# Performance work log

Measured on AMD Instinct MI355X. Metric: run time of the kernel, lower is better.

## Reference

```python
import jax, jax.numpy as jnp
import numpy as np

B, S, E, H = 4, 2048, 512, 1024

def setup_inputs() -> dict:
    key = jax.random.key(0)
    ks = jax.random.split(key, 8)
    s = 1.0 / np.sqrt(H)
    return {
        "hidden_states": jax.random.normal(ks[0], (B, S, H), jnp.float32),
        "external_embeddings": jax.random.normal(ks[1], (B, E, H), jnp.float32),
        "Wq": jax.random.normal(ks[2], (H, H), jnp.float32) * s,
        "bq": jax.random.normal(ks[3], (H,), jnp.float32) * 0.02,
        "Wk": jax.random.normal(ks[4], (H, H), jnp.float32) * s,
        "bk": jax.random.normal(ks[5], (H,), jnp.float32) * 0.02,
        "Wv": jax.random.normal(ks[6], (H, H), jnp.float32) * s,
        "bv": jax.random.normal(ks[7], (H,), jnp.float32) * 0.02,
    }

def reference(hidden_states, external_embeddings, Wq, bq, Wk, bk, Wv, bv):
    # Projections (torch Linear semantics: here weights stored as [in,out])
    q = hidden_states @ Wq + bq              # [B,S,H]
    k_tok = hidden_states @ Wk + bk          # [B,S,H]
    v_tok = hidden_states @ Wv + bv          # [B,S,H]
    k_ext = external_embeddings @ Wk + bk    # [B,E,H]
    v_ext = external_embeddings @ Wv + bv    # [B,E,H]
    # Each token attends to [its own key] ++ [external keys]; NO 1/sqrt(d) scaling
    # and NO head splitting, matching the original forward exactly.
    s_self = jnp.einsum('bsh,bsh->bs', q, k_tok)[..., None]   # [B,S,1]
    s_ext = jnp.einsum('bsh,beh->bse', q, k_ext)              # [B,S,E]
    scores = jnp.concatenate([s_self, s_ext], axis=-1)        # [B,S,1+E]
    probs = jax.nn.softmax(scores, axis=-1)
    ctx = probs[..., :1] * v_tok + jnp.einsum('bse,beh->bsh', probs[..., 1:], v_ext)
    return ctx  # [B,S,H]
```

## Files before the change

kernel.cpp:

```cpp
#include <hip/hip_runtime.h>
#include <stdint.h>

#define BB 4
#define SS 2048
#define EE 512
#define HH 1024

typedef _Float16 f16;
typedef __attribute__((ext_vector_type(8))) _Float16 f16x8;
typedef __attribute__((ext_vector_type(4))) _Float16 f16x4;
typedef __attribute__((ext_vector_type(4))) float f32x4;

__device__ __forceinline__ void async16(void* lds, const void* g) {
  __builtin_amdgcn_global_load_lds(
      (const __attribute__((address_space(1))) unsigned int*)g,
      (__attribute__((address_space(3))) unsigned int*)lds, 16, 0, 0);
}

template <int TERMS>
__device__ __forceinline__ void gemm_core(
    const f16* Ah, const f16* Al, const f16* Bh, const f16* Bl, int K, int ld,
    f16* lAh, f16* lAl, f16* lBh, f16* lBl, f32x4 acc[4][4]) {
  const int tid = threadIdx.x;
  const int wave = tid >> 6;
  const int lane = tid & 63;
  const int lrow = lane >> 2;
  const int lcol = (((lane & 3) ^ ((lane >> 3) & 3))) * 8;
  const int waveM = (wave >> 1) * 64;
  const int waveN = (wave & 1) * 64;
  const int frow = lane & 15;
  const int fk = ((lane >> 4) ^ ((frow >> 1) & 3)) * 8;

  for (int k0 = 0; k0 < K; k0 += 32) {
    __syncthreads();
#pragma unroll
    for (int i = 0; i < 2; ++i) {
      const int r0 = (wave * 2 + i) * 16;
      const size_t goff = (size_t)(r0 + lrow) * ld + (k0 + lcol);
      async16(&lAh[r0 * 32], Ah + goff);
      async16(&lBh[r0 * 32], Bh + goff);
      if (TERMS >= 2) async16(&lBl[r0 * 32], Bl + goff);
      if (TERMS >= 3) async16(&lAl[r0 * 32], Al + goff);
    }
    __syncthreads();

    f16x8 a[4], bh[4], bl[4], al[4];
#pragma unroll
    for (int i = 0; i < 4; ++i) {
      a[i] = *(const f16x8*)&lAh[(waveM + i * 16 + frow) * 32 + fk];
      bh[i] = *(const f16x8*)&lBh[(waveN + i * 16 + frow) * 32 + fk];
      if (TERMS >= 2) bl[i] = *(const f16x8*)&lBl[(waveN + i * 16 + frow) * 32 + fk];
      if (TERMS >= 3) al[i] = *(const f16x8*)&lAl[(waveM + i * 16 + frow) * 32 + fk];
    }
#pragma unroll
    for (int i = 0; i < 4; ++i)
#pragma unroll
      for (int j = 0; j < 4; ++j) {
        acc[i][j] = __builtin_amdgcn_mfma_f32_16x16x32_f16(a[i], bh[j], acc[i][j], 0, 0, 0);
        if (TERMS >= 2)
          acc[i][j] = __builtin_amdgcn_mfma_f32_16x16x32_f16(a[i], bl[j], acc[i][j], 0, 0, 0);
        if (TERMS >= 3)
          acc[i][j] = __builtin_amdgcn_mfma_f32_16x16x32_f16(al[i], bh[j], acc[i][j], 0, 0, 0);
      }
  }
}

__device__ __forceinline__ void epi_transposed(
    f16* __restrict__ dst, const f32x4 acc[4][4], const float bias[4], f16* tl) {
  const int tid = threadIdx.x, wave = tid >> 6, lane = tid & 63;
  const int waveM = (wave >> 1) * 64;
  const int colIn16 = lane & 15, quad = lane >> 4;
#pragma unroll
  for (int p = 0; p < 2; ++p) {
    __syncthreads();
    if ((wave & 1) == p) {
#pragma unroll
      for (int i = 0; i < 4; ++i)
#pragma unroll
        for (int j = 0; j < 4; ++j)
#pragma unroll
          for (int r = 0; r < 4; ++r) {
            const int row = waveM + i * 16 + quad * 4 + r;
            const int colL = j * 16 + colIn16;
            tl[colL * 136 + row] = (f16)(acc[i][j][r] + bias[j]);
          }
    }
    __syncthreads();
    for (int c = tid; c < 1024; c += 256) {
      const int colL = c >> 4, ch = c & 15;
      const f16x8 v = *(const f16x8*)&tl[colL * 136 + ch * 8];
      *(f16x8*)&dst[(size_t)(p * 64 + colL) * EE + ch * 8] = v;
    }
  }
}

__global__ __launch_bounds__(256) void cast_kernel(const float* __restrict__ xh32,
                                                   const float* __restrict__ xe32,
                                                   f16* __restrict__ xh,
                                                   f16* __restrict__ xe) {
  const int i = blockIdx.x * 256 + threadIdx.x;
  const int n4h = 8192 * HH / 4;
  const float* src = i < n4h ? xh32 : xe32;
  f16* dst = i < n4h ? xh : xe;
  const int k = i < n4h ? i : i - n4h;
  const float4 v = ((const float4*)src)[k];
  f16x4 o;
  o.x = (f16)v.x; o.y = (f16)v.y; o.z = (f16)v.z; o.w = (f16)v.w;
  ((f16x4*)dst)[k] = o;
}

__global__ void wsplit_kernel(const float* __restrict__ Wq, const float* __restrict__ Wk,
                              const float* __restrict__ Wv, f16* __restrict__ wt_hi,
                              f16* __restrict__ wt_lo) {
  __shared__ float tile[32][33];
  const int k0 = blockIdx.x * 32;
  const int n0g = blockIdx.y * 32;
  const int which = n0g >> 10;
  const float* W = which == 0 ? Wq : (which == 1 ? Wk : Wv);
  const int n0 = n0g & 1023;
  const int tx = threadIdx.x, ty = threadIdx.y;
#pragma unroll
  for (int i = 0; i < 32; i += 8)
    tile[ty + i][tx] = W[(size_t)(k0 + ty + i) * 1024 + n0 + tx];
  __syncthreads();
#pragma unroll
  for (int i = 0; i < 32; i += 8) {
    const int np = n0g + ty + i;
    const float v = tile[tx][ty + i];
    const size_t idx = (size_t)np * 1024 + k0 + tx;
    const f16 h = (f16)v;
    wt_hi[idx] = h;
    wt_lo[idx] = (f16)(v - (float)h);
  }
}

__global__ __launch_bounds__(256, 4) void proj_kernel(
    const f16* __restrict__ xh, const f16* __restrict__ xe,
    const f16* __restrict__ wt_hi, const f16* __restrict__ wt_lo,
    const float* __restrict__ bq, const float* __restrict__ bk,
    const float* __restrict__ bv, f16* __restrict__ q_hi, f16* __restrict__ q_lo,
    f16* __restrict__ kt, f16* __restrict__ vt,
    f16* __restrict__ ke_hi, f16* __restrict__ ke_lo, f16* __restrict__ veT) {
  const int g = blockIdx.x;
  const int j = g & 7;
  const int s = g >> 3;
  int mtile, ntile;
  if (s < 192) {
    const int w = s / 16, r = s % 16;
    ntile = w * 2 + (r & 1);
    mtile = (r >> 1) * 8 + j;
  } else {
    const int s2 = s - 192;
    const int w = s2 >> 2, r = s2 & 3;
    ntile = 8 + w * 2 + (r & 1);
    mtile = 64 + (r >> 1) * 8 + j;
  }
  const bool extRows = (mtile >= 64);

  __shared__ f16 lds[3 * 4096];

  const f16* A = extRows ? xe : xh;
  const int rowA = (extRows ? (mtile - 64) : mtile) * 128;
  const int rowB = ntile * 128;
  const bool split = (ntile < 8) || (extRows && ntile < 16);

  f32x4 acc[4][4];
#pragma unroll
  for (int i = 0; i < 4; ++i)
#pragma unroll
    for (int jj = 0; jj < 4; ++jj)
#pragma unroll
      for (int r = 0; r < 4; ++r) acc[i][jj][r] = 0.0f;

  if (split)
    gemm_core<2>(A + (size_t)rowA * HH, nullptr, wt_hi + (size_t)rowB * HH,
                 wt_lo + (size_t)rowB * HH, HH, HH,
                 lds, nullptr, lds + 4096, lds + 8192, acc);
  else
    gemm_core<1>(A + (size_t)rowA * HH, nullptr, wt_hi + (size_t)rowB * HH,
                 nullptr, HH, HH, lds, nullptr, lds + 4096, nullptr, acc);

  const int tid = threadIdx.x, wave = tid >> 6, lane = tid & 63;
  const int waveM = (wave >> 1) * 64, waveN = (wave & 1) * 64;
  const int colIn16 = lane & 15, rowQuad = (lane >> 4) * 4;
  float bias[4];
#pragma unroll
  for (int jj = 0; jj < 4; ++jj) {
    const int c = ntile * 128 + waveN + jj * 16 + colIn16;
    bias[jj] = c < 1024 ? bq[c] : (c < 2048 ? bk[c - 1024] : bv[c - 2048]);
  }

  if (extRows && ntile >= 16) {
    const int ge0 = (mtile - 64) * 128;
    const int bb = ge0 >> 9, e0 = ge0 & 511;
    epi_transposed(veT + ((size_t)bb * HH + (ntile - 16) * 128) * EE + e0,
                   acc, bias, lds);
    return;
  }

#pragma unroll
  for (int jj = 0; jj < 4; ++jj) {
    const int c = ntile * 128 + waveN + jj * 16 + colIn16;
#pragma unroll
    for (int i = 0; i < 4; ++i) {
#pragma unroll
      for (int r = 0; r < 4; ++r) {
        const int lrowIdx = waveM + i * 16 + rowQuad + r;
        const float val = acc[i][jj][r] + bias[jj];
        if (c < 1024) {
          const size_t idx = (size_t)(mtile * 128 + lrowIdx) * HH + c;
          const f16 h = (f16)val;
          q_hi[idx] = h;
          q_lo[idx] = (f16)(val - (float)h);
        } else if (c < 2048) {
          const int c2 = c - 1024;
          if (!extRows) {
            kt[(size_t)(mtile * 128 + lrowIdx) * HH + c2] = (f16)val;
          } else {
            const int ge = (mtile - 64) * 128 + lrowIdx;
            const size_t idx = (size_t)ge * HH + c2;
            const f16 h = (f16)val;
            ke_hi[idx] = h;
            ke_lo[idx] = (f16)(val - (float)h);
          }
        } else {
          vt[(size_t)(mtile * 128 + lrowIdx) * HH + (c - 2048)] = (f16)val;
        }
      }
    }
  }
}

__global__ __launch_bounds__(256, 4) void score_kernel(
    const f16* __restrict__ q_hi, const f16* __restrict__ q_lo,
    const f16* __restrict__ ke_hi, const f16* __restrict__ ke_lo,
    float* __restrict__ s_part) {
  const int b = blockIdx.z & 3;
  const int khalf = blockIdx.z >> 2;
  const int mtile = blockIdx.y;
  const int ntile = blockIdx.x;
  __shared__ f16 lds[4 * 4096];
  const size_t aoff = ((size_t)b * SS + mtile * 128) * HH + khalf * 512;
  const size_t boff = ((size_t)b * EE + ntile * 128) * HH + khalf * 512;

  f32x4 acc[4][4];
#pragma unroll
  for (int i = 0; i < 4; ++i)
#pragma unroll
    for (int j = 0; j < 4; ++j)
#pragma unroll
      for (int r = 0; r < 4; ++r) acc[i][j][r] = 0.0f;

  gemm_core<3>(q_hi + aoff, q_lo + aoff, ke_hi + boff, ke_lo + boff, 512, HH,
               lds, lds + 4096, lds + 8192, lds + 12288, acc);

  float* dst = s_part + (size_t)khalf * BB * SS * EE;
  const int tid = threadIdx.x, wave = tid >> 6, lane = tid & 63;
  const int waveM = (wave >> 1) * 64, waveN = (wave & 1) * 64;
  const int colIn16 = lane & 15, rowQuad = (lane >> 4) * 4;
#pragma unroll
  for (int j = 0; j < 4; ++j) {
    const int e = ntile * 128 + waveN + j * 16 + colIn16;
#pragma unroll
    for (int i = 0; i < 4; ++i)
#pragma unroll
      for (int r = 0; r < 4; ++r) {
        const int s = mtile * 128 + waveM + i * 16 + rowQuad + r;
        dst[((size_t)b * SS + s) * EE + e] = acc[i][j][r];
      }
  }
}

__global__ __launch_bounds__(256) void softmax_kernel(
    const f16* __restrict__ q_hi, const f16* __restrict__ q_lo,
    const f16* __restrict__ kt, const float* __restrict__ s_part,
    f16* __restrict__ probs, float* __restrict__ p_self) {
  const int t = blockIdx.x * 4 + (threadIdx.x >> 6);
  const int lane = threadIdx.x & 63;

  const size_t base = (size_t)t * HH;
  float ss = 0.f;
#pragma unroll
  for (int it = 0; it < 4; ++it) {
    const int off = it * 256 + lane * 4;
    const f16x4 qh = *(const f16x4*)&q_hi[base + off];
    const f16x4 ql = *(const f16x4*)&q_lo[base + off];
    const f16x4 kh = *(const f16x4*)&kt[base + off];
    ss += ((float)qh.x + (float)ql.x) * (float)kh.x;
    ss += ((float)qh.y + (float)ql.y) * (float)kh.y;
    ss += ((float)qh.z + (float)ql.z) * (float)kh.z;
    ss += ((float)qh.w + (float)ql.w) * (float)kh.w;
  }
#pragma unroll
  for (int m = 32; m > 0; m >>= 1) ss += __shfl_xor(ss, m, 64);

  const float* r0 = s_part + (size_t)t * EE;
  const float* r1 = s_part + (size_t)BB * SS * EE + (size_t)t * EE;
  const float4 a0 = *(const float4*)&r0[lane * 4];
  const float4 a1 = *(const float4*)&r0[256 + lane * 4];
  const float4 c0 = *(const float4*)&r1[lane * 4];
  const float4 c1 = *(const float4*)&r1[256 + lane * 4];
  const float v0x = a0.x + c0.x, v0y = a0.y + c0.y, v0z = a0.z + c0.z, v0w = a0.w + c0.w;
  const float v1x = a1.x + c1.x, v1y = a1.y + c1.y, v1z = a1.z + c1.z, v1w = a1.w + c1.w;
  float m = fmaxf(fmaxf(fmaxf(v0x, v0y), fmaxf(v0z, v0w)),
                  fmaxf(fmaxf(v1x, v1y), fmaxf(v1z, v1w)));
#pragma unroll
  for (int sh = 32; sh > 0; sh >>= 1) m = fmaxf(m, __shfl_xor(m, sh, 64));
  m = fmaxf(m, ss);
  const float e0 = __expf(v0x - m), e1 = __expf(v0y - m);
  const float e2 = __expf(v0z - m), e3 = __expf(v0w - m);
  const float e4 = __expf(v1x - m), e5 = __expf(v1y - m);
  const float e6 = __expf(v1z - m), e7 = __expf(v1w - m);
  float sum = ((e0 + e1) + (e2 + e3)) + ((e4 + e5) + (e6 + e7));
#pragma unroll
  for (int sh = 32; sh > 0; sh >>= 1) sum += __shfl_xor(sum, sh, 64);
  const float es = __expf(ss - m);
  const float inv = 1.0f / (sum + es);
  f16x4 p0, p1;
  p0.x = (f16)(e0 * inv); p0.y = (f16)(e1 * inv);
  p0.z = (f16)(e2 * inv); p0.w = (f16)(e3 * inv);
  p1.x = (f16)(e4 * inv); p1.y = (f16)(e5 * inv);
  p1.z = (f16)(e6 * inv); p1.w = (f16)(e7 * inv);
  *(f16x4*)&probs[(size_t)t * EE + lane * 4] = p0;
  *(f16x4*)&probs[(size_t)t * EE + 256 + lane * 4] = p1;
  if (lane == 0) p_self[t] = es * inv;
}

__global__ __launch_bounds__(256, 4) void pv_kernel(
    const f16* __restrict__ probs, const f16* __restrict__ veT,
    const float* __restrict__ p_self, const f16* __restrict__ vt,
    float* __restrict__ out) {
  const int b = blockIdx.z;
  const int mtile = blockIdx.y;
  const int ntile = blockIdx.x;
  __shared__ f16 lds[2 * 4096];
  const size_t aoff = ((size_t)b * SS + mtile * 128) * EE;
  const size_t boff = ((size_t)b * HH + ntile * 128) * EE;

  f32x4 acc[4][4];
#pragma unroll
  for (int i = 0; i < 4; ++i)
#pragma unroll
    for (int j = 0; j < 4; ++j)
#pragma unroll
      for (int r = 0; r < 4; ++r) acc[i][j][r] = 0.0f;

  gemm_core<1>(probs + aoff, nullptr, veT + boff, nullptr, EE, EE,
               lds, nullptr, lds + 4096, nullptr, acc);

  const int tid = threadIdx.x, wave = tid >> 6, lane = tid & 63;
  const int waveM = (wave >> 1) * 64, waveN = (wave & 1) * 64;
  const int colIn16 = lane & 15, rowQuad = (lane >> 4) * 4;
#pragma unroll
  for (int j = 0; j < 4; ++j) {
    const int h = ntile * 128 + waveN + j * 16 + colIn16;
#pragma unroll
    for (int i = 0; i < 4; ++i)
#pragma unroll
      for (int r = 0; r < 4; ++r) {
        const int s = mtile * 128 + waveM + i * 16 + rowQuad + r;
        const size_t t = (size_t)b * SS + s;
        __builtin_nontemporal_store(
            acc[i][j][r] + p_self[t] * (float)vt[t * HH + h], &out[t * HH + h]);
      }
  }
}

extern "C" void kernel_launch(void* const* d_in, const int* in_sizes, int n_in,
                              void* d_out, int out_size, void* d_ws, size_t ws_size,
                              hipStream_t stream) {
  const float* hidden = (const float*)d_in[0];
  const float* ext    = (const float*)d_in[1];
  const float* Wq = (const float*)d_in[2];
  const float* bq = (const float*)d_in[3];
  const float* Wk = (const float*)d_in[4];
  const float* bk = (const float*)d_in[5];
  const float* Wv = (const float*)d_in[6];
  const float* bv = (const float*)d_in[7];
  float* out = (float*)d_out;

  char* ws = (char*)d_ws;
  size_t off = 0;
  auto alloc = [&](size_t bytes) {
    char* p = ws + off;
    off += (bytes + 255) & ~(size_t)255;
    return p;
  };
  const size_t TOK = 8192, EXT = 2048;
  f16* xh    = (f16*)alloc(TOK * HH * 2);
  f16* xe    = (f16*)alloc(EXT * HH * 2);
  f16* wt_hi = (f16*)alloc(3072ull * HH * 2);
  f16* wt_lo = (f16*)alloc(3072ull * HH * 2);
  f16* q_hi  = (f16*)alloc(TOK * HH * 2);
  f16* q_lo  = (f16*)alloc(TOK * HH * 2);
  f16* kt    = (f16*)alloc(TOK * HH * 2);
  f16* vt    = (f16*)alloc(TOK * HH * 2);
  f16* ke_hi = (f16*)alloc(EXT * HH * 2);
  f16* ke_lo = (f16*)alloc(EXT * HH * 2);
  f16* veT   = (f16*)alloc((size_t)BB * HH * EE * 2);
  float* p_self = (float*)alloc(TOK * 4);
  float* s_part = (float*)alloc(2ull * BB * SS * EE * 4);
  f16* probs    = (f16*)alloc((size_t)BB * SS * EE * 2);

  cast_kernel<<<10240, 256, 0, stream>>>(hidden, ext, xh, xe);
  wsplit_kernel<<<dim3(32, 96), dim3(32, 8), 0, stream>>>(Wq, Wk, Wv, wt_hi, wt_lo);

  proj_kernel<<<1792, 256, 0, stream>>>(
      xh, xe, wt_hi, wt_lo, bq, bk, bv,
      q_hi, q_lo, kt, vt, ke_hi, ke_lo, veT);

  score_kernel<<<dim3(4, 16, 8), 256, 0, stream>>>(q_hi, q_lo, ke_hi, ke_lo, s_part);
  softmax_kernel<<<2048, 256, 0, stream>>>(q_hi, q_lo, kt, s_part, probs, p_self);
  pv_kernel<<<dim3(8, 16, 4), 256, 0, stream>>>(probs, veT, p_self, vt, out);
}
```

Baseline: 329.2 us.

## Rewrite projection GEMM with 256x256 tiles, 8 waves, and double-buffered async loads

The projection kernel moves from 128x128 tiles with 256 threads to 256x256 tiles with 512 threads and 448 blocks. The hi/lo split-weight product is now done as a K-loop that runs twice as long (the second half streams the low weights) rather than as two MFMAs per step. Global-to-LDS async loads are double-buffered and interleaved with MFMA phases using explicit waitcnt, barriers and setprio. The goal is more operand reuse per LDS load and overlap of memory with compute, at the cost of 128KB of LDS per block, more registers per thread, and fewer blocks in flight.

```diff
diff --git a/kernel.cpp b/kernel.cpp
--- a/kernel.cpp
+++ b/kernel.cpp
@@ -16,6 +16,8 @@
       (const __attribute__((address_space(1))) unsigned int*)g,
       (__attribute__((address_space(3))) unsigned int*)lds, 16, 0, 0);
 }
+
+#define MFMA16 __builtin_amdgcn_mfma_f32_16x16x32_f16
 
 template <int TERMS>
 __device__ __forceinline__ void gemm_core(
@@ -56,41 +58,12 @@
     for (int i = 0; i < 4; ++i)
 #pragma unroll
       for (int j = 0; j < 4; ++j) {
-        acc[i][j] = __builtin_amdgcn_mfma_f32_16x16x32_f16(a[i], bh[j], acc[i][j], 0, 0, 0);
+        acc[i][j] = MFMA16(a[i], bh[j], acc[i][j], 0, 0, 0);
         if (TERMS >= 2)
-          acc[i][j] = __builtin_amdgcn_mfma_f32_16x16x32_f16(a[i], bl[j], acc[i][j], 0, 0, 0);
+          acc[i][j] = MFMA16(a[i], bl[j], acc[i][j], 0, 0, 0);
         if (TERMS >= 3)
-          acc[i][j] = __builtin_amdgcn_mfma_f32_16x16x32_f16(al[i], bh[j], acc[i][j], 0, 0, 0);
-      }
-  }
-}
-
-__device__ __forceinline__ void epi_transposed(
-    f16* __restrict__ dst, const f32x4 acc[4][4], const float bias[4], f16* tl) {
-  const int tid = threadIdx.x, wave = tid >> 6, lane = tid & 63;
-  const int waveM = (wave >> 1) * 64;
-  const int colIn16 = lane & 15, quad = lane >> 4;
-#pragma unroll
-  for (int p = 0; p < 2; ++p) {
-    __syncthreads();
-    if ((wave & 1) == p) {
-#pragma unroll
-      for (int i = 0; i < 4; ++i)
-#pragma unroll
-        for (int j = 0; j < 4; ++j)
-#pragma unroll
-          for (int r = 0; r < 4; ++r) {
-            const int row = waveM + i * 16 + quad * 4 + r;
-            const int colL = j * 16 + colIn16;
-            tl[colL * 136 + row] = (f16)(acc[i][j][r] + bias[j]);
-          }
-    }
-    __syncthreads();
-    for (int c = tid; c < 1024; c += 256) {
-      const int colL = c >> 4, ch = c & 15;
-      const f16x8 v = *(const f16x8*)&tl[colL * 136 + ch * 8];
-      *(f16x8*)&dst[(size_t)(p * 64 + colL) * EE + ch * 8] = v;
-    }
+          acc[i][j] = MFMA16(al[i], bh[j], acc[i][j], 0, 0, 0);
+      }
   }
 }
 
@@ -134,7 +107,7 @@
   }
 }
 
-__global__ __launch_bounds__(256, 4) void proj_kernel(
+__global__ __launch_bounds__(512, 2) void proj_kernel(
     const f16* __restrict__ xh, const f16* __restrict__ xe,
     const f16* __restrict__ wt_hi, const f16* __restrict__ wt_lo,
     const float* __restrict__ bq, const float* __restrict__ bk,
@@ -144,87 +117,254 @@
   const int g = blockIdx.x;
   const int j = g & 7;
   const int s = g >> 3;
-  int mtile, ntile;
-  if (s < 192) {
-    const int w = s / 16, r = s % 16;
-    ntile = w * 2 + (r & 1);
-    mtile = (r >> 1) * 8 + j;
+  int mrow0, colB0;
+  bool ext = false, splitB = false;
+  if (s < 20) {
+    splitB = true;
+    if (s < 16) {
+      colB0 = (s >> 2) * 256;
+      mrow0 = ((s & 3) * 8 + j) * 256;
+    } else {
+      ext = true;
+      colB0 = 1024 + (s - 16) * 256;
+      mrow0 = j * 256;
+    }
   } else {
-    const int s2 = s - 192;
-    const int w = s2 >> 2, r = s2 & 3;
-    ntile = 8 + w * 2 + (r & 1);
-    mtile = 64 + (r >> 1) * 8 + j;
-  }
-  const bool extRows = (mtile >= 64);
-
-  __shared__ f16 lds[3 * 4096];
-
-  const f16* A = extRows ? xe : xh;
-  const int rowA = (extRows ? (mtile - 64) : mtile) * 128;
-  const int rowB = ntile * 128;
-  const bool split = (ntile < 8) || (extRows && ntile < 16);
-
-  f32x4 acc[4][4];
-#pragma unroll
-  for (int i = 0; i < 4; ++i)
+    const int s2 = s - 20;
+    if (s2 < 32) {
+      colB0 = (4 + (s2 >> 2)) * 256;
+      mrow0 = ((s2 & 3) * 8 + j) * 256;
+    } else {
+      ext = true;
+      colB0 = 1024 + (4 + (s2 - 32)) * 256;
+      mrow0 = j * 256;
+    }
+  }
+  const int NT = splitB ? 32 : 16;
+
+  __shared__ f16 lds[65536];
+
+  const int tid = threadIdx.x;
+  const int wave = tid >> 6, lane = tid & 63;
+  const int wm = wave >> 2, wn = wave & 3;
+  const int frow = lane & 15, qd = lane >> 4;
+
+  const f16* A0 = (ext ? xe : xh) + (size_t)mrow0 * HH;
+  const f16* Bhi = wt_hi + (size_t)colB0 * HH;
+  const f16* Blo = wt_lo + (size_t)colB0 * HH;
+
+  const int srow = tid >> 2;
+  const int scol = ((tid & 3) ^ ((srow >> 1) & 3)) * 8;
+  const size_t gO0 = (size_t)srow * HH + scol;
+  const size_t gO1 = (size_t)(128 + srow) * HH + scol;
+  const int ldst0 = (wave * 64) * 8;
+  const int ldst1 = (512 + wave * 64) * 8;
+
+  int offA[8], offB[4];
+#pragma unroll
+  for (int i = 0; i < 8; ++i) {
+    const int r = wm * 128 + i * 16 + frow;
+    offA[i] = r * 32 + ((qd ^ ((r >> 1) & 3)) * 8);
+  }
+#pragma unroll
+  for (int jj = 0; jj < 4; ++jj) {
+    const int r = wn * 64 + jj * 16 + frow;
+    offB[jj] = r * 32 + ((qd ^ ((r >> 1) & 3)) * 8);
+  }
+
+  f32x4 acc[8][4];
+#pragma unroll
+  for (int i = 0; i < 8; ++i)
 #pragma unroll
     for (int jj = 0; jj < 4; ++jj)
 #pragma unroll
       for (int r = 0; r < 4; ++r) acc[i][jj][r] = 0.0f;
 
-  if (split)
-    gemm_core<2>(A + (size_t)rowA * HH, nullptr, wt_hi + (size_t)rowB * HH,
-                 wt_lo + (size_t)rowB * HH, HH, HH,
-                 lds, nullptr, lds + 4096, lds + 8192, acc);
-  else
-    gemm_core<1>(A + (size_t)rowA * HH, nullptr, wt_hi + (size_t)rowB * HH,
-                 nullptr, HH, HH, lds, nullptr, lds + 4096, nullptr, acc);
-
-  const int tid = threadIdx.x, wave = tid >> 6, lane = tid & 63;
-  const int waveM = (wave >> 1) * 64, waveN = (wave & 1) * 64;
-  const int colIn16 = lane & 15, rowQuad = (lane >> 4) * 4;
+  {
+    f16* dA0 = &lds[0];
+    f16* dB0 = &lds[32768];
+    f16* dA1 = &lds[8192];
+    f16* dB1 = &lds[32768 + 8192];
+    async16(&dA0[ldst0], A0 + gO0);       async16(&dA0[ldst1], A0 + gO1);
+    async16(&dB0[ldst0], Bhi + gO0);      async16(&dB0[ldst1], Bhi + gO1);
+    async16(&dA1[ldst0], A0 + 32 + gO0);  async16(&dA1[ldst1], A0 + 32 + gO1);
+    async16(&dB1[ldst0], Bhi + 32 + gO0); async16(&dB1[ldst1], Bhi + 32 + gO1);
+  }
+  asm volatile("s_waitcnt vmcnt(4)" ::: "memory");
+  __builtin_amdgcn_s_barrier();
+
+  for (int t = 0; t < NT; ++t) {
+    const int cur = t & 1, nxt = cur ^ 1;
+    const bool st = (t + 1 < NT);
+    const int kn = ((t + 1) & 15) * 64;
+    const f16* An = A0 + kn;
+    const f16* Bn = (((t + 1) & 16) ? Blo : Bhi) + kn;
+    const f16* lA0 = &lds[(cur * 2 + 0) * 8192];
+    const f16* lB0 = &lds[32768 + (cur * 2 + 0) * 8192];
+    const f16* lA1 = &lds[(cur * 2 + 1) * 8192];
+    const f16* lB1 = &lds[32768 + (cur * 2 + 1) * 8192];
+    f16* sA0 = &lds[(nxt * 2 + 0) * 8192];
+    f16* sB0 = &lds[32768 + (nxt * 2 + 0) * 8192];
+    f16* sA1 = &lds[(nxt * 2 + 1) * 8192];
+    f16* sB1 = &lds[32768 + (nxt * 2 + 1) * 8192];
+
+    f16x8 a[8], b0, b1;
+
+#pragma unroll
+    for (int i = 0; i < 8; ++i) a[i] = *(const f16x8*)&lA0[offA[i]];
+    b0 = *(const f16x8*)&lB0[offB[0]];
+    b1 = *(const f16x8*)&lB0[offB[1]];
+    if (st) { async16(&sA0[ldst0], An + gO0); async16(&sA0[ldst1], An + gO1); }
+    __builtin_amdgcn_s_barrier();
+    __builtin_amdgcn_s_setprio(1);
+#pragma unroll
+    for (int i = 0; i < 8; ++i) {
+      acc[i][0] = MFMA16(a[i], b0, acc[i][0], 0, 0, 0);
+      acc[i][1] = MFMA16(a[i], b1, acc[i][1], 0, 0, 0);
+    }
+    __builtin_amdgcn_s_setprio(0);
+    __builtin_amdgcn_s_barrier();
+
+    b0 = *(const f16x8*)&lB0[offB[2]];
+    b1 = *(const f16x8*)&lB0[offB[3]];
+    if (st) { async16(&sB0[ldst0], Bn + gO0); async16(&sB0[ldst1], Bn + gO1); }
+    __builtin_amdgcn_s_barrier();
+    __builtin_amdgcn_s_setprio(1);
+#pragma unroll
+    for (int i = 0; i < 8; ++i) {
+      acc[i][2] = MFMA16(a[i], b0, acc[i][2], 0, 0, 0);
+      acc[i][3] = MFMA16(a[i], b1, acc[i][3], 0, 0, 0);
+    }
+    __builtin_amdgcn_s_setprio(0);
+    if (t == NT - 1) {
+      asm volatile("s_waitcnt vmcnt(0)" ::: "memory");
+    } else {
+      asm volatile("s_waitcnt vmcnt(4)" ::: "memory");
+    }
+    __builtin_amdgcn_s_barrier();
+
+#pragma unroll
+    for (int i = 0; i < 8; ++i) a[i] = *(const f16x8*)&lA1[offA[i]];
+    b0 = *(const f16x8*)&lB1[offB[0]];
+    b1 = *(const f16x8*)&lB1[offB[1]];
+    if (st) { async16(&sA1[ldst0], An + 32 + gO0); async16(&sA1[ldst1], An + 32 + gO1); }
+    __builtin_amdgcn_s_barrier();
+    __builtin_amdgcn_s_setprio(1);
+#pragma unroll
+    for (int i = 0; i < 8; ++i) {
+      acc[i][0] = MFMA16(a[i], b0, acc[i][0], 0, 0, 0);
+      acc[i][1] = MFMA16(a[i], b1, acc[i][1], 0, 0, 0);
+    }
+    __builtin_amdgcn_s_setprio(0);
+    __builtin_amdgcn_s_barrier();
+
+    b0 = *(const f16x8*)&lB1[offB[2]];
+    b1 = *(const f16x8*)&lB1[offB[3]];
+    if (st) { async16(&sB1[ldst0], Bn + 32 + gO0); async16(&sB1[ldst1], Bn + 32 + gO1); }
+    __builtin_amdgcn_s_barrier();
+    __builtin_amdgcn_s_setprio(1);
+#pragma unroll
+    for (int i = 0; i < 8; ++i) {
+      acc[i][2] = MFMA16(a[i], b0, acc[i][2], 0, 0, 0);
+      acc[i][3] = MFMA16(a[i], b1, acc[i][3], 0, 0, 0);
+    }
+    __builtin_amdgcn_s_setprio(0);
+    asm volatile("s_waitcnt vmcnt(4)" ::: "memory");
+    __builtin_amdgcn_s_barrier();
+  }
+
+  const int er0 = wm * 128 + qd * 4;
+  const int ec0 = wn * 64 + frow;
   float bias[4];
 #pragma unroll
   for (int jj = 0; jj < 4; ++jj) {
-    const int c = ntile * 128 + waveN + jj * 16 + colIn16;
+    const int c = colB0 + ec0 + jj * 16;
     bias[jj] = c < 1024 ? bq[c] : (c < 2048 ? bk[c - 1024] : bv[c - 2048]);
   }
 
-  if (extRows && ntile >= 16) {
-    const int ge0 = (mtile - 64) * 128;
-    const int bb = ge0 >> 9, e0 = ge0 & 511;
-    epi_transposed(veT + ((size_t)bb * HH + (ntile - 16) * 128) * EE + e0,
-                   acc, bias, lds);
-    return;
-  }
-
-#pragma unroll
-  for (int jj = 0; jj < 4; ++jj) {
-    const int c = ntile * 128 + waveN + jj * 16 + colIn16;
-#pragma unroll
-    for (int i = 0; i < 4; ++i) {
-#pragma unroll
-      for (int r = 0; r < 4; ++r) {
-        const int lrowIdx = waveM + i * 16 + rowQuad + r;
-        const float val = acc[i][jj][r] + bias[jj];
-        if (c < 1024) {
-          const size_t idx = (size_t)(mtile * 128 + lrowIdx) * HH + c;
-          const f16 h = (f16)val;
-          q_hi[idx] = h;
-          q_lo[idx] = (f16)(val - (float)h);
-        } else if (c < 2048) {
-          const int c2 = c - 1024;
-          if (!extRows) {
-            kt[(size_t)(mtile * 128 + lrowIdx) * HH + c2] = (f16)val;
-          } else {
-            const int ge = (mtile - 64) * 128 + lrowIdx;
-            const size_t idx = (size_t)ge * HH + c2;
+  if (!ext) {
+    if (colB0 < 1024) {
+#pragma unroll
+      for (int jj = 0; jj < 4; ++jj) {
+        const int c = colB0 + ec0 + jj * 16;
+#pragma unroll
+        for (int i = 0; i < 8; ++i)
+#pragma unroll
+          for (int r = 0; r < 4; ++r) {
+            const int row = mrow0 + er0 + i * 16 + r;
+            const float val = acc[i][jj][r] + bias[jj];
+            const size_t idx = (size_t)row * HH + c;
+            const f16 h = (f16)val;
+            q_hi[idx] = h;
+            q_lo[idx] = (f16)(val - (float)h);
+          }
+      }
+    } else if (colB0 < 2048) {
+#pragma unroll
+      for (int jj = 0; jj < 4; ++jj) {
+        const int c = colB0 + ec0 + jj * 16 - 1024;
+#pragma unroll
+        for (int i = 0; i < 8; ++i)
+#pragma unroll
+          for (int r = 0; r < 4; ++r) {
+            const int row = mrow0 + er0 + i * 16 + r;
+            kt[(size_t)row * HH + c] = (f16)(acc[i][jj][r] + bias[jj]);
+          }
+      }
+    } else {
+#pragma unroll
+      for (int jj = 0; jj < 4; ++jj) {
+        const int c = colB0 + ec0 + jj * 16 - 2048;
+#pragma unroll
+        for (int i = 0; i < 8; ++i)
+#pragma unroll
+          for (int r = 0; r < 4; ++r) {
+            const int row = mrow0 + er0 + i * 16 + r;
+            vt[(size_t)row * HH + c] = (f16)(acc[i][jj][r] + bias[jj]);
+          }
+      }
+    }
+  } else {
+    if (colB0 < 2048) {
+#pragma unroll
+      for (int jj = 0; jj < 4; ++jj) {
+        const int c = colB0 + ec0 + jj * 16 - 1024;
+#pragma unroll
+        for (int i = 0; i < 8; ++i)
+#pragma unroll
+          for (int r = 0; r < 4; ++r) {
+            const int row = mrow0 + er0 + i * 16 + r;
+            const float val = acc[i][jj][r] + bias[jj];
+            const size_t idx = (size_t)row * HH + c;
             const f16 h = (f16)val;
             ke_hi[idx] = h;
             ke_lo[idx] = (f16)(val - (float)h);
           }
-        } else {
-          vt[(size_t)(mtile * 128 + lrowIdx) * HH + (c - 2048)] = (f16)val;
+      }
+    } else {
+      f16* tl = lds;
+      const int b = mrow0 >> 9, e0 = mrow0 & 511;
+      const int h0 = colB0 - 2048;
+#pragma unroll
+      for (int p = 0; p < 2; ++p) {
+        __syncthreads();
+        if ((wn >> 1) == p) {
+          const int hL = (wn & 1) * 64 + frow;
+#pragma unroll
+          for (int jj = 0; jj < 4; ++jj)
+#pragma unroll
+            for (int i = 0; i < 8; ++i)
+#pragma unroll
+              for (int r = 0; r < 4; ++r) {
+                const int e = er0 + i * 16 + r;
+                tl[(hL + jj * 16) * 264 + e] = (f16)(acc[i][jj][r] + bias[jj]);
+              }
+        }
+        __syncthreads();
+        for (int c = tid; c < 128 * 32; c += 512) {
+          const int hL = c >> 5, ch = c & 31;
+          const f16x8 v = *(const f16x8*)&tl[hL * 264 + ch * 8];
+          *(f16x8*)&veT[(size_t)(b * HH + h0 + p * 128 + hL) * EE + e0 + ch * 8] = v;
         }
       }
     }
@@ -405,7 +545,7 @@
   cast_kernel<<<10240, 256, 0, stream>>>(hidden, ext, xh, xe);
   wsplit_kernel<<<dim3(32, 96), dim3(32, 8), 0, stream>>>(Wq, Wk, Wv, wt_hi, wt_lo);
 
-  proj_kernel<<<1792, 256, 0, stream>>>(
+  proj_kernel<<<448, 512, 0, stream>>>(
       xh, xe, wt_hi, wt_lo, bq, bk, bv,
       q_hi, q_lo, kt, vt, ke_hi, ke_lo, veT);
 
```

After: 306.1 us. 7.0% less time.
